# Kernel optimization log

Measured on AMD Instinct MI355X. Metric: run time of the kernel, lower is better.

The kernel has to match this reference:

```python
import jax, jax.numpy as jnp
import jax.lax as lax
import numpy as np
import math

B, T_FRAMES, H, W = 32, 8, 14, 14
C, CA = 768, 384
L = H * W + 1


def setup_inputs() -> dict:
    key = jax.random.key(0)
    ks = jax.random.split(key, 7)
    s = 0.02
    return {
        "x": jax.random.normal(ks[0], (B * T_FRAMES, L, C), dtype=jnp.float32),
        "W1": jax.random.normal(ks[1], (CA, C), dtype=jnp.float32) * s,
        "b1": jnp.zeros((CA,), dtype=jnp.float32),
        "conv_w": jax.random.normal(ks[2], (CA, 1, 3, 3, 3), dtype=jnp.float32) * s,
        "conv_b": jnp.zeros((CA,), dtype=jnp.float32),
        "W2": jax.random.normal(ks[3], (C, CA), dtype=jnp.float32) * s,
        "b2": jnp.zeros((C,), dtype=jnp.float32),
        "T": T_FRAMES,
    }


def reference(x, W1, b1, conv_w, conv_b, W2, b2, T):
    BT, Lx, Cx = x.shape
    Bb = BT // T
    Ca = W1.shape[0]
    Hh = Ww = int(round(math.sqrt(Lx - 1)))
    # fc1 on all tokens except CLS: [BT, L-1, Ca]
    h = jnp.einsum("blc,ac->bla", x[:, 1:, :], W1) + b1
    # -> [B, Ca, T, H, W] for depthwise 3d conv (groups = Ca)
    h = h.reshape(Bb, T, Hh, Ww, Ca).transpose(0, 4, 1, 2, 3)
    h = lax.conv_general_dilated(
        h, conv_w,
        window_strides=(1, 1, 1),
        padding=[(1, 1), (1, 1), (1, 1)],
        dimension_numbers=("NCDHW", "OIDHW", "NCDHW"),
        feature_group_count=Ca,
    ) + conv_b[None, :, None, None, None]
    # back to [BT, L-1, Ca]
    h = h.transpose(0, 2, 3, 4, 1).reshape(BT, Lx - 1, Ca)
    # fc2: [BT, L-1, C]
    h = jnp.einsum("bla,ca->blc", h, W2) + b2
    # residual add onto non-CLS tokens
    return x.at[:, 1:, :].add(h)
```

## Files before the change

### kernel.cpp

```cpp
#include <hip/hip_runtime.h>
#include <hip/hip_bf16.h>
#include <stdint.h>

#define BTOT   256
#define LX     197
#define CDIM   768
#define CADIM  384
#define TFR    8
#define LM1    196
#define MTOT   50176

typedef unsigned short u16;
typedef short          bf16x8 __attribute__((ext_vector_type(8)));
typedef unsigned short u16x4  __attribute__((ext_vector_type(4)));
typedef unsigned short u16x8  __attribute__((ext_vector_type(8)));
typedef float          f32x4  __attribute__((ext_vector_type(4)));

typedef const __attribute__((address_space(1))) void gvoid_t;
typedef __attribute__((address_space(3))) void       svoid_t;

static __device__ __forceinline__ u16 f2bf(float f) {
  union { float f; uint32_t u; } v; v.f = f;
  uint32_t u = v.u;
  return (u16)((u + 0x7FFFu + ((u >> 16) & 1u)) >> 16);
}
static __device__ __forceinline__ float bf2f(u16 h) {
  union { uint32_t u; float f; } v; v.u = ((uint32_t)h) << 16;
  return v.f;
}
static __device__ __forceinline__ u16 f2bf_hw(float f) {
  union { __hip_bfloat16 b; u16 u; } v;
  v.b = __float2bfloat16(f);
  return v.u;
}

__global__ void prep_small(const float4* __restrict__ x4, float4* __restrict__ out4,
                           const float* __restrict__ W1, const float* __restrict__ W2,
                           const float* __restrict__ cw, u16* __restrict__ w1b,
                           u16* __restrict__ w2b, float* __restrict__ cwT) {
  int i = blockIdx.x * blockDim.x + threadIdx.x;
  if (i < CADIM * CDIM) { w1b[i] = f2bf(W1[i]); w2b[i] = f2bf(W2[i]); }
  if (i < CADIM * 27) {
    int a = i / 27; int tap = i - a * 27;
    cwT[tap * CADIM + a] = cw[i];
  }
  if (i < BTOT * 192) {
    int f = i / 192, v = i - f * 192;
    size_t off = (size_t)f * (LX * CDIM / 4) + v;
    out4[off] = x4[off];
  }
}


#define GEMM_STAGE2(bufidx, k0)                                            \
  {                                                                        \
    _Pragma("unroll")                                                      \
    for (int s = 0; s < 2; ++s) {                                          \
      __builtin_amdgcn_global_load_lds((gvoid_t*)(A + aoff[s] + (k0)),     \
          (svoid_t*)(As + (bufidx) * 4096 + ldst[s]), 16, 0, 0);           \
      __builtin_amdgcn_global_load_lds((gvoid_t*)(Bw + boff[s] + (k0)),    \
          (svoid_t*)(Bs + (bufidx) * 4096 + ldst[s]), 16, 0, 0);           \
    }                                                                      \
  }

#define GEMM_COMPUTE(bufidx)                                               \
  {                                                                        \
    const u16* Ab = As + (bufidx) * 4096;                                  \
    const u16* Bb = Bs + (bufidx) * 4096;                                  \
    bf16x8 af[4], bfr[4];                                                  \
    _Pragma("unroll")                                                      \
    for (int i = 0; i < 4; i++) af[i] = *(const bf16x8*)&Ab[abase + i * 512]; \
    _Pragma("unroll")                                                      \
    for (int j = 0; j < 4; j++) bfr[j] = *(const bf16x8*)&Bb[bbase + j * 512]; \
    _Pragma("unroll")                                                      \
    for (int i = 0; i < 4; i++)                                            \
      _Pragma("unroll")                                                    \
      for (int j = 0; j < 4; j++)                                          \
        acc[i][j] = __builtin_amdgcn_mfma_f32_16x16x32_bf16(af[i], bfr[j], acc[i][j], 0, 0, 0); \
  }

__global__ __launch_bounds__(768, 2) void fc1_gemm(
    const float* __restrict__ X,
    const u16* __restrict__ Bw,
    const float* __restrict__ bias,
    u16* __restrict__ Hout)
{
  __shared__ __align__(16) u16 As[2 * 128 * 32];
  __shared__ __align__(16) u16 Bs[2 * 384 * 32];
  const int tid  = threadIdx.x;
  const int lane = tid & 63;
  const int wave = tid >> 6;
  const int m0 = blockIdx.x * 128;
  const int lm = lane & 15;
  const int lk = lane >> 4;
  const int wr = wave / 6;
  const int wc = wave - wr * 6;
  const int wm = wr * 64;
  const int wn = wc * 64;
  const bool is_a = (wave < 4);

  const int g = tid >> 3;
  const int q = tid & 7;
  size_t arow[4];
  int awst[4];
  if (is_a) {
#pragma unroll
    for (int s = 0; s < 4; ++s) {
      int row = g + 32 * s;
      int tok = m0 + row;
      int bt = tok / LM1;
      int l  = tok - bt * LM1;
      arow[s] = (size_t)(bt * LX + 1 + l) * CDIM + q * 4;
      int R    = row >> 1;
      int uu   = (row & 1) * 4 + (q >> 1);
      int slot = uu ^ (R & 7);
      awst[s]  = R * 64 + slot * 8 + (q & 1) * 4;
    }
  }

  const int wb  = wave - 4;
  const int u   = (lane & 7) ^ (lane >> 3);
  const int rr  = 2 * (lane >> 3) + (u >> 2);
  const int cko = (u & 3) * 8;
  size_t boff[3];
  int ldst[3];
  if (!is_a) {
#pragma unroll
    for (int s = 0; s < 3; ++s) {
      int row = wb * 48 + s * 16 + rr;
      boff[s] = (size_t)row * CDIM + cko;
      ldst[s] = (wb * 24 + s * 8) * 64;
    }
  }

  const int lmh   = lm >> 1;
  const int slotp = (((lm & 1) << 2) | lk) ^ lmh;
  const int abase = ((wm >> 1) + lmh) * 64 + slotp * 8;
  const int bbase = ((wn >> 1) + lmh) * 64 + slotp * 8;

  f32x4 acc[4][4];
#pragma unroll
  for (int i = 0; i < 4; i++)
#pragma unroll
    for (int j = 0; j < 4; j++) acc[i][j] = (f32x4)0.0f;

  float4 areg[4];

  if (is_a) {
#pragma unroll
    for (int s = 0; s < 4; ++s) areg[s] = *(const float4*)(X + arow[s]);
#pragma unroll
    for (int s = 0; s < 4; ++s) {
      u16x4 o;
      o[0] = f2bf_hw(areg[s].x); o[1] = f2bf_hw(areg[s].y);
      o[2] = f2bf_hw(areg[s].z); o[3] = f2bf_hw(areg[s].w);
      *(u16x4*)&As[awst[s]] = o;
    }
  } else {
#pragma unroll
    for (int s = 0; s < 3; ++s)
      __builtin_amdgcn_global_load_lds((gvoid_t*)(Bw + boff[s]),
          (svoid_t*)(Bs + ldst[s]), 16, 0, 0);
  }
  __syncthreads();

  int cur = 0;
  for (int kt = 0; kt < 23; ++kt) {
    const int k1 = (kt + 1) * 32;
    const int nb = cur ^ 1;
    if (is_a) {
#pragma unroll
      for (int s = 0; s < 4; ++s) areg[s] = *(const float4*)(X + arow[s] + k1);
    } else {
#pragma unroll
      for (int s = 0; s < 3; ++s)
        __builtin_amdgcn_global_load_lds((gvoid_t*)(Bw + boff[s] + k1),
            (svoid_t*)(Bs + nb * 12288 + ldst[s]), 16, 0, 0);
    }
    {
      const u16* Ab = As + cur * 4096;
      const u16* Bb = Bs + cur * 12288;
      bf16x8 af[4], bfr[4];
#pragma unroll
      for (int i = 0; i < 4; i++) af[i] = *(const bf16x8*)&Ab[abase + i * 512];
#pragma unroll
      for (int j = 0; j < 4; j++) bfr[j] = *(const bf16x8*)&Bb[bbase + j * 512];
#pragma unroll
      for (int i = 0; i < 4; i++)
#pragma unroll
        for (int j = 0; j < 4; j++)
          acc[i][j] = __builtin_amdgcn_mfma_f32_16x16x32_bf16(af[i], bfr[j], acc[i][j], 0, 0, 0);
    }
    if (is_a) {
#pragma unroll
      for (int s = 0; s < 4; ++s) {
        u16x4 o;
        o[0] = f2bf_hw(areg[s].x); o[1] = f2bf_hw(areg[s].y);
        o[2] = f2bf_hw(areg[s].z); o[3] = f2bf_hw(areg[s].w);
        *(u16x4*)&As[nb * 4096 + awst[s]] = o;
      }
    }
    __syncthreads();
    cur ^= 1;
  }
  {
    const u16* Ab = As + cur * 4096;
    const u16* Bb = Bs + cur * 12288;
    bf16x8 af[4], bfr[4];
#pragma unroll
    for (int i = 0; i < 4; i++) af[i] = *(const bf16x8*)&Ab[abase + i * 512];
#pragma unroll
    for (int j = 0; j < 4; j++) bfr[j] = *(const bf16x8*)&Bb[bbase + j * 512];
#pragma unroll
    for (int i = 0; i < 4; i++)
#pragma unroll
      for (int j = 0; j < 4; j++)
        acc[i][j] = __builtin_amdgcn_mfma_f32_16x16x32_bf16(af[i], bfr[j], acc[i][j], 0, 0, 0);
  }

#pragma unroll
  for (int i = 0; i < 4; i++) {
    int rbase = m0 + wm + i * 16 + lk * 4;
#pragma unroll
    for (int j = 0; j < 4; j++) {
      int col = wn + j * 16 + lm;
      float bv = bias[col];
#pragma unroll
      for (int r = 0; r < 4; r++)
        Hout[(rbase + r) * CADIM + col] = f2bf(acc[i][j][r] + bv);
    }
  }
}

__global__ __launch_bounds__(256) void dwconv(
    const u16* __restrict__ h1, const float* __restrict__ cwT,
    const float* __restrict__ cb, u16* __restrict__ h2)
{
  int idx = blockIdx.x * blockDim.x + threadIdx.x;
  int cg = idx % 48;
  int rest = idx / 48;
  int wp = rest % 7; rest /= 7;
  int hp = rest % 7; rest /= 7;
  int t = rest & 7;
  int frame = rest;
  int a0 = cg * 8;
  int h0 = hp * 2, w0 = wp * 2;

  float acc[2][2][8];
#pragma unroll
  for (int c = 0; c < 8; ++c) {
    float bv = cb[a0 + c];
    acc[0][0][c] = bv; acc[0][1][c] = bv; acc[1][0][c] = bv; acc[1][1][c] = bv;
  }

#pragma unroll
  for (int dt = -1; dt <= 1; ++dt) {
    int tt = t + dt;
    if (tt < 0 || tt >= TFR) continue;
    float wreg[9][8];
#pragma unroll
    for (int j = 0; j < 9; ++j) {
      const float* wp8 = cwT + ((dt + 1) * 9 + j) * CADIM + a0;
#pragma unroll
      for (int c = 0; c < 8; ++c) wreg[j][c] = wp8[c];
    }
    const u16* fbase = h1 + (size_t)(frame + dt) * LM1 * CADIM + a0;
#pragma unroll
    for (int ih = 0; ih < 4; ++ih) {
      int hh = h0 - 1 + ih;
      if (hh < 0 || hh >= 14) continue;
#pragma unroll
      for (int iw = 0; iw < 4; ++iw) {
        int ww = w0 - 1 + iw;
        if (ww < 0 || ww >= 14) continue;
        bf16x8 v = *(const bf16x8*)(fbase + (hh * 14 + ww) * CADIM);
        float vf[8];
#pragma unroll
        for (int c = 0; c < 8; ++c) vf[c] = bf2f((u16)v[c]);
#pragma unroll
        for (int oh = 0; oh < 2; ++oh) {
          if (ih - 1 - oh < -1 || ih - 1 - oh > 1) continue;
#pragma unroll
          for (int ow = 0; ow < 2; ++ow) {
            if (iw - 1 - ow < -1 || iw - 1 - ow > 1) continue;
            int j = (ih - oh) * 3 + (iw - ow);
#pragma unroll
            for (int c = 0; c < 8; ++c)
              acc[oh][ow][c] += vf[c] * wreg[j][c];
          }
        }
      }
    }
  }
  const size_t obase = (size_t)frame * LM1 * CADIM + a0;
#pragma unroll
  for (int oh = 0; oh < 2; ++oh)
#pragma unroll
    for (int ow = 0; ow < 2; ++ow) {
      u16x8 o;
#pragma unroll
      for (int c = 0; c < 8; ++c) o[c] = f2bf(acc[oh][ow][c]);
      *(u16x8*)(h2 + obase + ((size_t)(h0 + oh) * 14 + w0 + ow) * CADIM) = o;
    }
}

__global__ __launch_bounds__(256) void fc2_gemm(
    const u16* __restrict__ A,
    const u16* __restrict__ Bw,
    const float* __restrict__ bias,
    const float* __restrict__ x,
    float* __restrict__ out)
{
  __shared__ __align__(16) u16 As[2 * 128 * 32];
  __shared__ __align__(16) u16 Bs[2 * 128 * 32];
  const int tid  = threadIdx.x;
  const int lane = tid & 63;
  const int wave = tid >> 6;
  const int m0 = blockIdx.x * 128;
  const int n0 = blockIdx.y * 128;
  const int lm = lane & 15;
  const int lk = lane >> 4;
  const int wm = (wave & 1) * 64;
  const int wn = (wave >> 1) * 64;

  const int u   = (lane & 7) ^ (lane >> 3);
  const int rr  = 2 * (lane >> 3) + (u >> 2);
  const int cko = (u & 3) * 8;
  size_t aoff[2], boff[2];
  int ldst[2];
#pragma unroll
  for (int s = 0; s < 2; ++s) {
    int row = wave * 32 + s * 16 + rr;
    aoff[s] = (size_t)(m0 + row) * CADIM + cko;
    boff[s] = (size_t)(n0 + row) * CADIM + cko;
    ldst[s] = (wave * 16 + s * 8) * 64;
  }

  const int lmh   = lm >> 1;
  const int slotp = (((lm & 1) << 2) | lk) ^ lmh;
  const int abase = ((wm >> 1) + lmh) * 64 + slotp * 8;
  const int bbase = ((wn >> 1) + lmh) * 64 + slotp * 8;

  f32x4 acc[4][4];
#pragma unroll
  for (int i = 0; i < 4; i++)
#pragma unroll
    for (int j = 0; j < 4; j++) acc[i][j] = (f32x4)0.0f;

  GEMM_STAGE2(0, 0);
  __syncthreads();
  int cur = 0;
  for (int kt = 0; kt < 11; ++kt) {
    GEMM_STAGE2(cur ^ 1, (kt + 1) * 32);
    GEMM_COMPUTE(cur);
    __syncthreads();
    cur ^= 1;
  }
  GEMM_COMPUTE(cur);

  float bv[4];
#pragma unroll
  for (int j = 0; j < 4; j++) bv[j] = bias[n0 + wn + j * 16 + lm];
#pragma unroll
  for (int i = 0; i < 4; i++) {
    int rbase = m0 + wm + i * 16 + lk * 4;
    size_t orow[4];
#pragma unroll
    for (int r = 0; r < 4; r++) {
      int tok = rbase + r;
      int bt = tok / LM1;
      int l  = tok - bt * LM1;
      orow[r] = (size_t)(bt * LX + 1 + l) * CDIM + (n0 + wn + lm);
    }
    float xv[4][4];
#pragma unroll
    for (int r = 0; r < 4; r++)
#pragma unroll
      for (int j = 0; j < 4; j++)
        xv[r][j] = x[orow[r] + j * 16];
#pragma unroll
    for (int r = 0; r < 4; r++)
#pragma unroll
      for (int j = 0; j < 4; j++)
        out[orow[r] + j * 16] = xv[r][j] + acc[i][j][r] + bv[j];
  }
}

extern "C" void kernel_launch(void* const* d_in, const int* in_sizes, int n_in,
                              void* d_out, int out_size, void* d_ws, size_t ws_size,
                              hipStream_t stream) {
  const float* x  = (const float*)d_in[0];
  const float* W1 = (const float*)d_in[1];
  const float* b1 = (const float*)d_in[2];
  const float* cw = (const float*)d_in[3];
  const float* cb = (const float*)d_in[4];
  const float* W2 = (const float*)d_in[5];
  const float* b2 = (const float*)d_in[6];
  float* out = (float*)d_out;

  char* ws = (char*)d_ws;
  u16*   w1b = (u16*)(ws + 0);
  u16*   w2b = (u16*)(ws + 589824);
  float* cwT = (float*)(ws + 1179648);
  u16*   h1  = (u16*)(ws + 1245184);
  u16*   h2  = (u16*)(ws + 39780352);

  prep_small<<<1152, 256, 0, stream>>>((const float4*)x, (float4*)out,
                                       W1, W2, cw, w1b, w2b, cwT);
  fc1_gemm<<<MTOT / 128, 768, 0, stream>>>(x, w1b, b1, h1);
  dwconv  <<<(BTOT * 49 * 48) / 256, 256, 0, stream>>>(h1, cwT, cb, h2);
  fc2_gemm<<<dim3(MTOT / 128, CDIM / 128), 256, 0, stream>>>(h2, w2b, b2, x, out);
}
```

Baseline: 446.0 us.

## Stage dwconv frames in LDS and widen fc2 tiles to 128x384

The depthwise conv now stages three adjacent frames for a 32-channel slice in shared memory, so each block covers a whole frame instead of each thread re-reading overlapping neighbours from global memory. fc2 moves to 768-thread blocks with a 128x384 output tile, using specialised loader waves for A and B, which cuts redundant A reloads from six column tiles down to two. The trade-off is more shared memory per block and fewer blocks for the conv, which could lower occupancy.

```diff
diff --git a/kernel.cpp b/kernel.cpp
--- a/kernel.cpp
+++ b/kernel.cpp
@@ -51,33 +51,6 @@
   }
 }
 
-
-#define GEMM_STAGE2(bufidx, k0)                                            \
-  {                                                                        \
-    _Pragma("unroll")                                                      \
-    for (int s = 0; s < 2; ++s) {                                          \
-      __builtin_amdgcn_global_load_lds((gvoid_t*)(A + aoff[s] + (k0)),     \
-          (svoid_t*)(As + (bufidx) * 4096 + ldst[s]), 16, 0, 0);           \
-      __builtin_amdgcn_global_load_lds((gvoid_t*)(Bw + boff[s] + (k0)),    \
-          (svoid_t*)(Bs + (bufidx) * 4096 + ldst[s]), 16, 0, 0);           \
-    }                                                                      \
-  }
-
-#define GEMM_COMPUTE(bufidx)                                               \
-  {                                                                        \
-    const u16* Ab = As + (bufidx) * 4096;                                  \
-    const u16* Bb = Bs + (bufidx) * 4096;                                  \
-    bf16x8 af[4], bfr[4];                                                  \
-    _Pragma("unroll")                                                      \
-    for (int i = 0; i < 4; i++) af[i] = *(const bf16x8*)&Ab[abase + i * 512]; \
-    _Pragma("unroll")                                                      \
-    for (int j = 0; j < 4; j++) bfr[j] = *(const bf16x8*)&Bb[bbase + j * 512]; \
-    _Pragma("unroll")                                                      \
-    for (int i = 0; i < 4; i++)                                            \
-      _Pragma("unroll")                                                    \
-      for (int j = 0; j < 4; j++)                                          \
-        acc[i][j] = __builtin_amdgcn_mfma_f32_16x16x32_bf16(af[i], bfr[j], acc[i][j], 0, 0, 0); \
-  }
 
 __global__ __launch_bounds__(768, 2) void fc1_gemm(
     const float* __restrict__ X,
@@ -236,75 +209,82 @@
     const u16* __restrict__ h1, const float* __restrict__ cwT,
     const float* __restrict__ cb, u16* __restrict__ h2)
 {
-  int idx = blockIdx.x * blockDim.x + threadIdx.x;
-  int cg = idx % 48;
-  int rest = idx / 48;
-  int wp = rest % 7; rest /= 7;
-  int hp = rest % 7; rest /= 7;
-  int t = rest & 7;
-  int frame = rest;
-  int a0 = cg * 8;
-  int h0 = hp * 2, w0 = wp * 2;
-
-  float acc[2][2][8];
-#pragma unroll
-  for (int c = 0; c < 8; ++c) {
-    float bv = cb[a0 + c];
-    acc[0][0][c] = bv; acc[0][1][c] = bv; acc[1][0][c] = bv; acc[1][1][c] = bv;
-  }
-
-#pragma unroll
-  for (int dt = -1; dt <= 1; ++dt) {
-    int tt = t + dt;
-    if (tt < 0 || tt >= TFR) continue;
-    float wreg[9][8];
+  __shared__ __align__(16) u16 lin[3 * 196 * 32];
+  const int tid = threadIdx.x;
+  const int f   = blockIdx.x;
+  const int cc  = blockIdx.y;
+  const int tv  = f & 7;
+
+  for (int i = tid; i < 3 * 196 * 4; i += 256) {
+    int fd  = i / 784;
+    int rem = i - fd * 784;
+    int pos = rem >> 2;
+    int c8  = rem & 3;
+    int tt  = tv + fd - 1;
+    u16x8 v = (u16x8)0;
+    if (tt >= 0 && tt < TFR) {
+      const u16* src = h1 + ((size_t)(f + fd - 1) * LM1 + pos) * CADIM
+                          + cc * 32 + c8 * 8;
+      v = *(const u16x8*)src;
+    }
+    *(u16x8*)&lin[(fd * 196 + pos) * 32 + c8 * 8] = v;
+  }
+  __syncthreads();
+
+  const int cg    = tid & 3;
+  const int pidx  = tid >> 2;
+  const int cbase = cc * 32 + cg * 8;
+
+  float bv[8];
+#pragma unroll
+  for (int c = 0; c < 8; ++c) bv[c] = cb[cbase + c];
+
+  float acc[4][8];
+  int hk[4], wk[4];
+#pragma unroll
+  for (int k = 0; k < 4; ++k) {
+    int p = pidx + 64 * k;
+    hk[k] = p / 14;
+    wk[k] = p - hk[k] * 14;
+#pragma unroll
+    for (int c = 0; c < 8; ++c) acc[k][c] = bv[c];
+  }
+
+  for (int dt = 0; dt < 3; ++dt) {
 #pragma unroll
     for (int j = 0; j < 9; ++j) {
-      const float* wp8 = cwT + ((dt + 1) * 9 + j) * CADIM + a0;
-#pragma unroll
-      for (int c = 0; c < 8; ++c) wreg[j][c] = wp8[c];
-    }
-    const u16* fbase = h1 + (size_t)(frame + dt) * LM1 * CADIM + a0;
-#pragma unroll
-    for (int ih = 0; ih < 4; ++ih) {
-      int hh = h0 - 1 + ih;
-      if (hh < 0 || hh >= 14) continue;
-#pragma unroll
-      for (int iw = 0; iw < 4; ++iw) {
-        int ww = w0 - 1 + iw;
-        if (ww < 0 || ww >= 14) continue;
-        bf16x8 v = *(const bf16x8*)(fbase + (hh * 14 + ww) * CADIM);
-        float vf[8];
-#pragma unroll
-        for (int c = 0; c < 8; ++c) vf[c] = bf2f((u16)v[c]);
-#pragma unroll
-        for (int oh = 0; oh < 2; ++oh) {
-          if (ih - 1 - oh < -1 || ih - 1 - oh > 1) continue;
-#pragma unroll
-          for (int ow = 0; ow < 2; ++ow) {
-            if (iw - 1 - ow < -1 || iw - 1 - ow > 1) continue;
-            int j = (ih - oh) * 3 + (iw - ow);
-#pragma unroll
-            for (int c = 0; c < 8; ++c)
-              acc[oh][ow][c] += vf[c] * wreg[j][c];
-          }
-        }
+      const int dh = j / 3 - 1, dw = j % 3 - 1;
+      float w8[8];
+      const float* wp8 = cwT + (dt * 9 + j) * CADIM + cbase;
+#pragma unroll
+      for (int c = 0; c < 8; ++c) w8[c] = wp8[c];
+#pragma unroll
+      for (int k = 0; k < 4; ++k) {
+        int p = pidx + 64 * k;
+        if (p >= 196) continue;
+        int hh = hk[k] + dh, ww = wk[k] + dw;
+        if (hh < 0 || hh >= 14 || ww < 0 || ww >= 14) continue;
+        const u16x8 v = *(const u16x8*)&lin[(dt * 196 + hh * 14 + ww) * 32 + cg * 8];
+#pragma unroll
+        for (int c = 0; c < 8; ++c)
+          acc[k][c] += bf2f((u16)v[c]) * w8[c];
       }
     }
   }
-  const size_t obase = (size_t)frame * LM1 * CADIM + a0;
-#pragma unroll
-  for (int oh = 0; oh < 2; ++oh)
-#pragma unroll
-    for (int ow = 0; ow < 2; ++ow) {
+
+#pragma unroll
+  for (int k = 0; k < 4; ++k) {
+    int p = pidx + 64 * k;
+    if (p < 196) {
       u16x8 o;
 #pragma unroll
-      for (int c = 0; c < 8; ++c) o[c] = f2bf(acc[oh][ow][c]);
-      *(u16x8*)(h2 + obase + ((size_t)(h0 + oh) * 14 + w0 + ow) * CADIM) = o;
-    }
-}
-
-__global__ __launch_bounds__(256) void fc2_gemm(
+      for (int c = 0; c < 8; ++c) o[c] = f2bf(acc[k][c]);
+      *(u16x8*)(h2 + ((size_t)f * LM1 + p) * CADIM + cbase) = o;
+    }
+  }
+}
+
+__global__ __launch_bounds__(768, 2) void fc2_gemm(
     const u16* __restrict__ A,
     const u16* __restrict__ Bw,
     const float* __restrict__ bias,
@@ -312,28 +292,44 @@
     float* __restrict__ out)
 {
   __shared__ __align__(16) u16 As[2 * 128 * 32];
-  __shared__ __align__(16) u16 Bs[2 * 128 * 32];
+  __shared__ __align__(16) u16 Bs[2 * 384 * 32];
   const int tid  = threadIdx.x;
   const int lane = tid & 63;
   const int wave = tid >> 6;
   const int m0 = blockIdx.x * 128;
-  const int n0 = blockIdx.y * 128;
+  const int n0 = blockIdx.y * 384;
   const int lm = lane & 15;
   const int lk = lane >> 4;
-  const int wm = (wave & 1) * 64;
-  const int wn = (wave >> 1) * 64;
+  const int wr = wave / 6;
+  const int wc = wave - wr * 6;
+  const int wm = wr * 64;
+  const int wn = wc * 64;
+  const bool is_a = (wave < 4);
 
   const int u   = (lane & 7) ^ (lane >> 3);
   const int rr  = 2 * (lane >> 3) + (u >> 2);
   const int cko = (u & 3) * 8;
-  size_t aoff[2], boff[2];
-  int ldst[2];
-#pragma unroll
-  for (int s = 0; s < 2; ++s) {
-    int row = wave * 32 + s * 16 + rr;
-    aoff[s] = (size_t)(m0 + row) * CADIM + cko;
-    boff[s] = (size_t)(n0 + row) * CADIM + cko;
-    ldst[s] = (wave * 16 + s * 8) * 64;
+
+  size_t aoff[2];
+  int lasta[2];
+  if (is_a) {
+#pragma unroll
+    for (int s = 0; s < 2; ++s) {
+      int row = wave * 32 + s * 16 + rr;
+      aoff[s]  = (size_t)(m0 + row) * CADIM + cko;
+      lasta[s] = (wave * 16 + s * 8) * 64;
+    }
+  }
+  const int wb = wave - 4;
+  size_t boff[3];
+  int ldst[3];
+  if (!is_a) {
+#pragma unroll
+    for (int s = 0; s < 3; ++s) {
+      int row = wb * 48 + s * 16 + rr;
+      boff[s] = (size_t)(n0 + row) * CADIM + cko;
+      ldst[s] = (wb * 24 + s * 8) * 64;
+    }
   }
 
   const int lmh   = lm >> 1;
@@ -347,20 +343,69 @@
 #pragma unroll
     for (int j = 0; j < 4; j++) acc[i][j] = (f32x4)0.0f;
 
-  GEMM_STAGE2(0, 0);
+  if (is_a) {
+#pragma unroll
+    for (int s = 0; s < 2; ++s)
+      __builtin_amdgcn_global_load_lds((gvoid_t*)(A + aoff[s]),
+          (svoid_t*)(As + lasta[s]), 16, 0, 0);
+  } else {
+#pragma unroll
+    for (int s = 0; s < 3; ++s)
+      __builtin_amdgcn_global_load_lds((gvoid_t*)(Bw + boff[s]),
+          (svoid_t*)(Bs + ldst[s]), 16, 0, 0);
+  }
   __syncthreads();
+
   int cur = 0;
   for (int kt = 0; kt < 11; ++kt) {
-    GEMM_STAGE2(cur ^ 1, (kt + 1) * 32);
-    GEMM_COMPUTE(cur);
+    const int k1 = (kt + 1) * 32;
+    const int nb = cur ^ 1;
+    if (is_a) {
+#pragma unroll
+      for (int s = 0; s < 2; ++s)
+        __builtin_amdgcn_global_load_lds((gvoid_t*)(A + aoff[s] + k1),
+            (svoid_t*)(As + nb * 4096 + lasta[s]), 16, 0, 0);
+    } else {
+#pragma unroll
+      for (int s = 0; s < 3; ++s)
+        __builtin_amdgcn_global_load_lds((gvoid_t*)(Bw + boff[s] + k1),
+            (svoid_t*)(Bs + nb * 12288 + ldst[s]), 16, 0, 0);
+    }
+    {
+      const u16* Ab = As + cur * 4096;
+      const u16* Bb = Bs + cur * 12288;
+      bf16x8 af[4], bfr[4];
+#pragma unroll
+      for (int i = 0; i < 4; i++) af[i] = *(const bf16x8*)&Ab[abase + i * 512];
+#pragma unroll
+      for (int j = 0; j < 4; j++) bfr[j] = *(const bf16x8*)&Bb[bbase + j * 512];
+#pragma unroll
+      for (int i = 0; i < 4; i++)
+#pragma unroll
+        for (int j = 0; j < 4; j++)
+          acc[i][j] = __builtin_amdgcn_mfma_f32_16x16x32_bf16(af[i], bfr[j], acc[i][j], 0, 0, 0);
+    }
     __syncthreads();
     cur ^= 1;
   }
-  GEMM_COMPUTE(cur);
-
-  float bv[4];
-#pragma unroll
-  for (int j = 0; j < 4; j++) bv[j] = bias[n0 + wn + j * 16 + lm];
+  {
+    const u16* Ab = As + cur * 4096;
+    const u16* Bb = Bs + cur * 12288;
+    bf16x8 af[4], bfr[4];
+#pragma unroll
+    for (int i = 0; i < 4; i++) af[i] = *(const bf16x8*)&Ab[abase + i * 512];
+#pragma unroll
+    for (int j = 0; j < 4; j++) bfr[j] = *(const bf16x8*)&Bb[bbase + j * 512];
+#pragma unroll
+    for (int i = 0; i < 4; i++)
+#pragma unroll
+      for (int j = 0; j < 4; j++)
+        acc[i][j] = __builtin_amdgcn_mfma_f32_16x16x32_bf16(af[i], bfr[j], acc[i][j], 0, 0, 0);
+  }
+
+  float bve[4];
+#pragma unroll
+  for (int j = 0; j < 4; j++) bve[j] = bias[n0 + wn + j * 16 + lm];
 #pragma unroll
   for (int i = 0; i < 4; i++) {
     int rbase = m0 + wm + i * 16 + lk * 4;
@@ -382,7 +427,7 @@
     for (int r = 0; r < 4; r++)
 #pragma unroll
       for (int j = 0; j < 4; j++)
-        out[orow[r] + j * 16] = xv[r][j] + acc[i][j][r] + bv[j];
+        out[orow[r] + j * 16] = xv[r][j] + acc[i][j][r] + bve[j];
   }
 }
 
@@ -408,6 +453,6 @@
   prep_small<<<1152, 256, 0, stream>>>((const float4*)x, (float4*)out,
                                        W1, W2, cw, w1b, w2b, cwT);
   fc1_gemm<<<MTOT / 128, 768, 0, stream>>>(x, w1b, b1, h1);
-  dwconv  <<<(BTOT * 49 * 48) / 256, 256, 0, stream>>>(h1, cwT, cb, h2);
-  fc2_gemm<<<dim3(MTOT / 128, CDIM / 128), 256, 0, stream>>>(h2, w2b, b2, x, out);
-}
+  dwconv  <<<dim3(BTOT, 12), 256, 0, stream>>>(h1, cwT, cb, h2);
+  fc2_gemm<<<dim3(MTOT / 128, 2), 768, 0, stream>>>(h2, w2b, b2, x, out);
+}
```

Result: no change. 452.3 us (+1.4%).
